# Kernel optimization log

Measured on AMD Instinct MI355X. Metric: run time of the kernel, lower is better.

The kernel has to match this reference:

```python
import jax, jax.numpy as jnp
import numpy as np

SHAPES = ((64, 64), (32, 32), (16, 16), (8, 8))
HEADS, LV, P = 8, 4, 8


def _ln(x, g, b, eps=1e-5):
    m = x.mean(-1, keepdims=True)
    v = ((x - m) ** 2).mean(-1, keepdims=True)
    return (x - m) * jax.lax.rsqrt(v + eps) * g + b


def _sample_level(v, H, W, loc):
    # v: [B, heads, H*W, hd] value for one level; loc: [B, L, heads, P, 2] in [0,1]
    # Matches F.grid_sample(mode='bilinear', padding_mode='zeros', align_corners=False)
    x = loc[..., 0] * W - 0.5
    y = loc[..., 1] * H - 0.5
    x0 = jnp.floor(x)
    y0 = jnp.floor(y)
    B, L, hds, Pn = x.shape
    acc = 0.0
    for dx, dy in ((0, 0), (1, 0), (0, 1), (1, 1)):
        xi = x0 + dx
        yi = y0 + dy
        w = (1.0 - jnp.abs(x - xi)) * (1.0 - jnp.abs(y - yi))
        valid = (xi >= 0) & (xi < W) & (yi >= 0) & (yi < H)
        idx = (jnp.clip(yi, 0, H - 1) * W + jnp.clip(xi, 0, W - 1)).astype(jnp.int32)
        idx_r = idx.transpose(0, 2, 1, 3).reshape(B, hds, L * Pn)  # [B,heads,L*P]
        g = jnp.take_along_axis(v, idx_r[..., None], axis=2)  # [B,heads,L*P,hd]
        g = g.reshape(B, hds, L, Pn, -1).transpose(0, 2, 1, 3, 4)  # [B,L,heads,P,hd]
        acc = acc + (w * valid.astype(w.dtype))[..., None] * g
    return acc


def setup_inputs() -> dict:
    key = jax.random.key(0)
    ks = iter(jax.random.split(key, 64))
    B, d, depth, dff = 2, 256, 6, 1024
    inp = {}
    for i, (H, W) in enumerate(SHAPES):
        inp[f"src{i}"] = jax.random.normal(next(ks), (B, d, H, W), jnp.float32)
        inp[f"pos{i}"] = jax.random.normal(next(ks), (B, d, H, W), jnp.float32)
    s = 0.02
    off_dim = HEADS * LV * P * 2  # 512
    aw_dim = HEADS * LV * P  # 256
    inp["level_embed"] = jax.random.normal(next(ks), (LV, d), jnp.float32)
    inp["W_off"] = jax.random.normal(next(ks), (depth, d, off_dim), jnp.float32) * s
    inp["b_off"] = jax.random.normal(next(ks), (depth, off_dim), jnp.float32) * 0.5
    inp["W_attn"] = jax.random.normal(next(ks), (depth, d, aw_dim), jnp.float32) * s
    inp["b_attn"] = jnp.zeros((depth, aw_dim), jnp.float32)
    inp["W_val"] = jax.random.normal(next(ks), (depth, d, d), jnp.float32) * s
    inp["b_val"] = jnp.zeros((depth, d), jnp.float32)
    inp["W_out"] = jax.random.normal(next(ks), (depth, d, d), jnp.float32) * s
    inp["b_out"] = jnp.zeros((depth, d), jnp.float32)
    inp["ln1_g"] = jnp.ones((depth, d), jnp.float32)
    inp["ln1_b"] = jnp.zeros((depth, d), jnp.float32)
    inp["W1"] = jax.random.normal(next(ks), (depth, d, dff), jnp.float32) * s
    inp["b1"] = jnp.zeros((depth, dff), jnp.float32)
    inp["W2"] = jax.random.normal(next(ks), (depth, dff, d), jnp.float32) * s
    inp["b2"] = jnp.zeros((depth, d), jnp.float32)
    inp["ln2_g"] = jnp.ones((depth, d), jnp.float32)
    inp["ln2_b"] = jnp.zeros((depth, d), jnp.float32)
    return inp


def reference(src0, src1, src2, src3, pos0, pos1, pos2, pos3, level_embed,
              W_off, b_off, W_attn, b_attn, W_val, b_val, W_out, b_out,
              ln1_g, ln1_b, W1, b1, W2, b2, ln2_g, ln2_b):
    srcs = [src0, src1, src2, src3]
    poss = [pos0, pos1, pos2, pos3]
    B, d = src0.shape[0], src0.shape[1]
    hd = d // HEADS
    # flatten multi-scale maps: [B, C, H, W] -> [B, H*W, C]
    src_flat = jnp.concatenate([s.reshape(B, d, -1).transpose(0, 2, 1) for s in srcs], 1)
    pos_flat = jnp.concatenate(
        [p.reshape(B, d, -1).transpose(0, 2, 1) + level_embed[i] for i, p in enumerate(poss)], 1)
    # reference points; masks are all-False so valid_ratios == 1 (same ref for every level)
    refs = []
    for (H, W) in SHAPES:
        gy, gx = jnp.meshgrid((jnp.arange(H) + 0.5) / H, (jnp.arange(W) + 0.5) / W, indexing='ij')
        refs.append(jnp.stack([gx.reshape(-1), gy.reshape(-1)], -1))
    ref = jnp.concatenate(refs, 0)  # [L, 2]
    norm = jnp.array([[W, H] for (H, W) in SHAPES], jnp.float32)  # [LV, 2] (W_, H_)
    sizes = [H * W for (H, W) in SHAPES]
    starts = np.cumsum([0] + sizes[:-1]).tolist()
    depth = W_off.shape[0]
    L = src_flat.shape[1]
    x = src_flat
    for i in range(depth):
        # pre-norm deformable self-attention; value comes from un-normed residual stream
        x2 = _ln(x, ln1_g[i], ln1_b[i])
        q = x2 + pos_flat
        off = (q @ W_off[i] + b_off[i]).reshape(B, L, HEADS, LV, P, 2)
        attn = jax.nn.softmax((q @ W_attn[i] + b_attn[i]).reshape(B, L, HEADS, LV * P), -1)
        attn = attn.reshape(B, L, HEADS, LV, P)
        val = (x @ W_val[i] + b_val[i]).reshape(B, L, HEADS, hd).transpose(0, 2, 1, 3)  # [B,heads,L,hd]
        loc = ref[None, :, None, None, None, :] + off / norm[None, None, None, :, None, :]
        out = 0.0
        for l, (H, W) in enumerate(SHAPES):
            vl = val[:, :, starts[l]:starts[l] + sizes[l]]
            sl = _sample_level(vl, H, W, loc[:, :, :, l])  # [B,L,heads,P,hd]
            out = out + (attn[:, :, :, l, :, None] * sl).sum(3)
        out = out.reshape(B, L, d) @ W_out[i] + b_out[i]
        x = x + out
        # pre-norm FFN with exact gelu (torch default)
        x2 = _ln(x, ln2_g[i], ln2_b[i])
        x = x + jax.nn.gelu(x2 @ W1[i] + b1[i], approximate=False) @ W2[i] + b2[i]
    return x
```

## Files before the change

kernel.cpp:

```cpp
#include <hip/hip_runtime.h>
#include <hip/hip_bf16.h>
#include <math.h>

#define L_TOK 5440
#define NTOK  10880
#define D     256

typedef __attribute__((ext_vector_type(8))) short short8;
typedef __attribute__((ext_vector_type(4))) short short4v;
typedef __attribute__((ext_vector_type(4))) float f32x4;

__device__ __forceinline__ short f2bf(float f) {
    __hip_bfloat16 h = __float2bfloat16(f);
    return __builtin_bit_cast(short, h);
}
__device__ __forceinline__ float bf2f(short s) {
    unsigned u = ((unsigned)(unsigned short)s) << 16;
    return __builtin_bit_cast(float, u);
}

#define GLL16(gp, lp) \
    __builtin_amdgcn_global_load_lds((const __attribute__((address_space(1))) void*)(gp), \
                                     (__attribute__((address_space(3))) void*)(lp), 16, 0, 0)

__global__ __launch_bounds__(256) void flat_kernel(
    const float* __restrict__ s, const float* __restrict__ p, const float* __restrict__ le,
    float* __restrict__ x, short* __restrict__ xb, float* __restrict__ pos,
    int HW, int start, int lv)
{
    __shared__ float ts[32][33], tp[32][33];
    int b = blockIdx.z, c0 = blockIdx.y * 32, pix0 = blockIdx.x * 32;
    int tx = threadIdx.x & 31, ty = threadIdx.x >> 5;
#pragma unroll
    for (int i = 0; i < 4; ++i) {
        int c = c0 + ty + i * 8;
        size_t gi = ((size_t)b * D + c) * HW + pix0 + tx;
        ts[ty + i * 8][tx] = s[gi];
        tp[ty + i * 8][tx] = p[gi];
    }
    __syncthreads();
#pragma unroll
    for (int i = 0; i < 4; ++i) {
        int pix = pix0 + ty + i * 8;
        size_t bl = (size_t)b * L_TOK + start + pix;
        int c = c0 + tx;
        float v = ts[tx][ty + i * 8];
        x[bl * D + c]   = v;
        xb[bl * D + c]  = f2bf(v);
        pos[bl * D + c] = tp[tx][ty + i * 8] + le[lv * D + c];
    }
}

__global__ __launch_bounds__(256) void wconv_kernel(
    const float* __restrict__ W, short* __restrict__ Wt, int K, int N,
    int dstride, int rowoff)
{
    __shared__ float tile[32][33];
    int d = blockIdx.z;
    int n0 = blockIdx.x * 32, k0 = blockIdx.y * 32;
    const float* Wd = W + (size_t)d * K * N;
    short* Wtd = Wt + (size_t)d * dstride + (size_t)rowoff * K;
    int tx = threadIdx.x & 31, ty = threadIdx.x >> 5;
#pragma unroll
    for (int i = 0; i < 4; ++i)
        tile[ty + i * 8][tx] = Wd[(size_t)(k0 + ty + i * 8) * N + n0 + tx];
    __syncthreads();
#pragma unroll
    for (int i = 0; i < 4; ++i)
        Wtd[(size_t)(n0 + ty + i * 8) * K + k0 + tx] = f2bf(tile[tx][ty + i * 8]);
}

__global__ __launch_bounds__(256) void bpack_kernel(
    const float* __restrict__ boff, const float* __restrict__ batt, float* __restrict__ bqa)
{
    int i = blockIdx.x * 256 + threadIdx.x;
    if (i >= 6 * 768) return;
    int d = i / 768, c = i - d * 768;
    bqa[i] = (c < 512) ? boff[d * 512 + c] : batt[d * 256 + c - 512];
}

__global__ __launch_bounds__(256) void ln_kernel(
    const float* __restrict__ x, const float* __restrict__ g, const float* __restrict__ bta,
    const float* __restrict__ pos, short* __restrict__ out)
{
    int wid = threadIdx.x >> 6, lane = threadIdx.x & 63;
    int m = blockIdx.x * 4 + wid;
    const float* xr = x + (size_t)m * D;
    float v[4];
#pragma unroll
    for (int i = 0; i < 4; ++i) v[i] = xr[lane + i * 64];
    float s = v[0] + v[1] + v[2] + v[3];
#pragma unroll
    for (int o = 32; o; o >>= 1) s += __shfl_xor(s, o);
    float mean = s * (1.0f / D);
    float sq = 0.0f;
#pragma unroll
    for (int i = 0; i < 4; ++i) { float d = v[i] - mean; sq += d * d; }
#pragma unroll
    for (int o = 32; o; o >>= 1) sq += __shfl_xor(sq, o);
    float rstd = rsqrtf(sq * (1.0f / D) + 1e-5f);
    short* orow = out + (size_t)m * D;
#pragma unroll
    for (int i = 0; i < 4; ++i) {
        int c = lane + i * 64;
        float o = (v[i] - mean) * rstd * g[c] + bta[c];
        if (pos) o += pos[(size_t)m * D + c];
        orow[c] = f2bf(o);
    }
}

template<int BN>
__device__ __forceinline__ void mm_body64(
    const short* __restrict__ A, const short* __restrict__ Wt,
    const float* __restrict__ bias, const float* __restrict__ resid,
    float* __restrict__ Cf, short* __restrict__ Cb,
    int row0, int col0, int K, int ldc, int act)
{
    constexpr int NW  = BN / 4;
    constexpr int NF  = NW / 16;
    constexpr int BCH = BN / 32;
    __shared__ __align__(16) short As[2][64 * 64];
    __shared__ __align__(16) short Bs[2][BN * 64];
    int tid = threadIdx.x, lane = tid & 63, w = tid >> 6;
    int l15 = lane & 15, l16 = lane >> 4;

    int a_off[4][2], b_off[NF][2];
#pragma unroll
    for (int m = 0; m < 4; ++m)
#pragma unroll
        for (int kk = 0; kk < 2; ++kk) {
            int ra = m * 16 + l15;
            a_off[m][kk] = ra * 64 + (((kk * 4 + l16) ^ (ra & 7)) << 3);
        }
#pragma unroll
    for (int n = 0; n < NF; ++n)
#pragma unroll
        for (int kk = 0; kk < 2; ++kk) {
            int rb = w * NW + n * 16 + l15;
            b_off[n][kk] = rb * 64 + (((kk * 4 + l16) ^ (rb & 7)) << 3);
        }

    int sg = (lane & 7) ^ ((lane >> 3) & 7);
    const short* ag = A  + (size_t)(row0 + w * 16 + (lane >> 3)) * K + sg * 8;
    const short* bg = Wt + (size_t)(col0 + w * NW + (lane >> 3)) * K + sg * 8;

    f32x4 acc[4][NF];
#pragma unroll
    for (int m = 0; m < 4; ++m)
#pragma unroll
        for (int n = 0; n < NF; ++n) acc[m][n] = (f32x4){0.f, 0.f, 0.f, 0.f};

    auto stage = [&](int buf, int kofs) {
#pragma unroll
        for (int c = 0; c < 2; ++c)
            GLL16(ag + (size_t)c * 8 * K + kofs, &As[buf][w * 1024 + c * 512]);
#pragma unroll
        for (int c = 0; c < BCH; ++c)
            GLL16(bg + (size_t)c * 8 * K + kofs, &Bs[buf][w * NW * 64 + c * 512]);
    };
    auto comp = [&](int buf) {
#pragma unroll
        for (int kk = 0; kk < 2; ++kk) {
            short8 af[4], bfr[NF];
#pragma unroll
            for (int m = 0; m < 4; ++m) af[m] = *(short8*)&As[buf][a_off[m][kk]];
#pragma unroll
            for (int n = 0; n < NF; ++n) bfr[n] = *(short8*)&Bs[buf][b_off[n][kk]];
#pragma unroll
            for (int m = 0; m < 4; ++m)
#pragma unroll
                for (int n = 0; n < NF; ++n)
                    acc[m][n] = __builtin_amdgcn_mfma_f32_16x16x32_bf16(af[m], bfr[n], acc[m][n], 0, 0, 0);
        }
    };

    stage(0, 0);
    __syncthreads();
    int cur = 0;
    for (int k0 = 64; k0 < K; k0 += 64) {
        stage(cur ^ 1, k0);
        comp(cur);
        __syncthreads();
        cur ^= 1;
    }
    comp(cur);

#pragma unroll
    for (int m = 0; m < 4; ++m) {
#pragma unroll
        for (int j = 0; j < 4; ++j) {
            int row = row0 + m * 16 + l16 * 4 + j;
#pragma unroll
            for (int n = 0; n < NF; ++n) {
                int col = col0 + w * NW + n * 16 + l15;
                float v = acc[m][n][j] + bias[col];
                if (act) v = 0.5f * v * (1.0f + erff(v * 0.70710678118654752f));
                if (resid) v += resid[(size_t)row * ldc + col];
                if (Cf) Cf[(size_t)row * ldc + col] = v;
                if (Cb) Cb[(size_t)row * ldc + col] = f2bf(v);
            }
        }
    }
}

template<int BN>
__global__ __launch_bounds__(256) void mm_kernel(
    const short* __restrict__ A, const short* __restrict__ Wt,
    const float* __restrict__ bias, const float* __restrict__ resid,
    float* __restrict__ Cf, short* __restrict__ Cb, int K, int ldc, int act)
{
    mm_body64<BN>(A, Wt, bias, resid, Cf, Cb, blockIdx.y * 64, blockIdx.x * BN, K, ldc, act);
}

__global__ __launch_bounds__(256) void mm2_kernel(
    const short* __restrict__ A1, const short* __restrict__ Wt1, const float* __restrict__ bias1,
    float* __restrict__ Cf1, int ldc1,
    const short* __restrict__ A2, const short* __restrict__ Wt2, const float* __restrict__ bias2,
    short* __restrict__ Cb2, int ldc2,
    int nx1, int K)
{
    const short *A, *Wt; const float* bias; float* Cf; short* Cb; int ldc, col0;
    if ((int)blockIdx.x < nx1) {
        A = A1; Wt = Wt1; bias = bias1; Cf = Cf1; Cb = nullptr; ldc = ldc1;
        col0 = blockIdx.x * 128;
    } else {
        A = A2; Wt = Wt2; bias = bias2; Cf = nullptr; Cb = Cb2; ldc = ldc2;
        col0 = (blockIdx.x - nx1) * 128;
    }
    mm_body64<128>(A, Wt, bias, nullptr, Cf, Cb, blockIdx.y * 64, col0, K, ldc, 0);
}

__global__ __launch_bounds__(256) void sample_kernel(
    const float* __restrict__ big, const short* __restrict__ val, short* __restrict__ out)
{
    __shared__ float sw[8 * 132];
    __shared__ int   si[8 * 132];
    int bl = blockIdx.x;
    int b = bl / L_TOK, l = bl - b * L_TOK;
    const float* row = big + (size_t)bl * 768;
    int t = threadIdx.x;
    {
        int head = t >> 5, lvp = t & 31, lv = lvp >> 3, p = lvp & 7;
        int lq, r;
        if (l < 4096)      { lq = 0; r = l;        }
        else if (l < 5120) { lq = 1; r = l - 4096; }
        else if (l < 5376) { lq = 2; r = l - 5120; }
        else               { lq = 3; r = l - 5376; }
        int sh = 6 - lq;
        float invSq = 1.0f / (float)(1 << sh);
        float refx = ((r & ((1 << sh) - 1)) + 0.5f) * invSq;
        float refy = ((r >> sh) + 0.5f) * invSq;
        int S = 64 >> lv;
        int start = (lv == 0) ? 0 : (lv == 1) ? 4096 : (lv == 2) ? 5120 : 5376;
        float Sf = (float)S;
        float logit = row[512 + head * 32 + lvp];
        float mx = logit;
#pragma unroll
        for (int o = 16; o; o >>= 1) mx = fmaxf(mx, __shfl_xor(mx, o));
        float e = __expf(logit - mx);
        float ssum = e;
#pragma unroll
        for (int o = 16; o; o >>= 1) ssum += __shfl_xor(ssum, o);
        float a = e / ssum;
        float ox = row[head * 64 + lv * 16 + p * 2 + 0];
        float oy = row[head * 64 + lv * 16 + p * 2 + 1];
        float X = refx * Sf + ox - 0.5f;
        float Y = refy * Sf + oy - 0.5f;
        float x0 = floorf(X), y0 = floorf(Y);
        float fx = X - x0, fy = Y - y0;
        int xi0 = (int)x0, yi0 = (int)y0;
        int qt = lvp >> 3, sidx = lvp & 7;
        int base_w = head * 132 + qt * 33 + sidx * 4;
#pragma unroll
        for (int tap = 0; tap < 4; ++tap) {
            int dx = tap & 1, dy = tap >> 1;
            int xi = xi0 + dx, yi = yi0 + dy;
            float wgt = (dx ? fx : 1.0f - fx) * (dy ? fy : 1.0f - fy);
            bool valid = (xi >= 0) && (xi < S) && (yi >= 0) && (yi < S);
            int xc = xi < 0 ? 0 : (xi > S - 1 ? S - 1 : xi);
            int yc = yi < 0 ? 0 : (yi > S - 1 ? S - 1 : yi);
            sw[base_w + tap] = valid ? wgt * a : 0.0f;
            si[base_w + tap] = start + yc * S + xc;
        }
    }
    __syncthreads();
    int h = t >> 5, sgp = (t >> 2) & 7, cg = t & 3;
    const short* vb = val + (size_t)b * L_TOK * D + h * 32 + cg * 8;
    float a0 = 0.f, a1 = 0.f, a2 = 0.f, a3 = 0.f;
    float a4 = 0.f, a5 = 0.f, a6 = 0.f, a7 = 0.f;
#pragma unroll
    for (int ss = 0; ss < 4; ++ss) {
        int base = h * 132 + ss * 33 + sgp * 4;
#pragma unroll
        for (int tap = 0; tap < 4; ++tap) {
            float wgt = sw[base + tap];
            int   idx = si[base + tap];
            const short8 g = *(const short8*)&vb[(size_t)idx * D];
            a0 += wgt * bf2f(g[0]); a1 += wgt * bf2f(g[1]);
            a2 += wgt * bf2f(g[2]); a3 += wgt * bf2f(g[3]);
            a4 += wgt * bf2f(g[4]); a5 += wgt * bf2f(g[5]);
            a6 += wgt * bf2f(g[6]); a7 += wgt * bf2f(g[7]);
        }
    }
#pragma unroll
    for (int o = 4; o <= 16; o <<= 1) {
        a0 += __shfl_xor(a0, o); a1 += __shfl_xor(a1, o);
        a2 += __shfl_xor(a2, o); a3 += __shfl_xor(a3, o);
        a4 += __shfl_xor(a4, o); a5 += __shfl_xor(a5, o);
        a6 += __shfl_xor(a6, o); a7 += __shfl_xor(a7, o);
    }
    if (sgp == 0) {
        short8 o;
        o[0] = f2bf(a0); o[1] = f2bf(a1); o[2] = f2bf(a2); o[3] = f2bf(a3);
        o[4] = f2bf(a4); o[5] = f2bf(a5); o[6] = f2bf(a6); o[7] = f2bf(a7);
        *(short8*)&out[(size_t)bl * D + h * 32 + cg * 8] = o;
    }
}

extern "C" void kernel_launch(void* const* d_in, const int* in_sizes, int n_in,
                              void* d_out, int out_size, void* d_ws, size_t ws_size,
                              hipStream_t stream)
{
    const float* s0    = (const float*)d_in[0];
    const float* p0    = (const float*)d_in[1];
    const float* s1    = (const float*)d_in[2];
    const float* p1    = (const float*)d_in[3];
    const float* s2    = (const float*)d_in[4];
    const float* p2    = (const float*)d_in[5];
    const float* s3    = (const float*)d_in[6];
    const float* p3    = (const float*)d_in[7];
    const float* lvl   = (const float*)d_in[8];
    const float* W_off = (const float*)d_in[9];
    const float* b_off = (const float*)d_in[10];
    const float* W_att = (const float*)d_in[11];
    const float* b_att = (const float*)d_in[12];
    const float* W_val = (const float*)d_in[13];
    const float* b_val = (const float*)d_in[14];
    const float* W_out = (const float*)d_in[15];
    const float* b_out = (const float*)d_in[16];
    const float* ln1g  = (const float*)d_in[17];
    const float* ln1b  = (const float*)d_in[18];
    const float* W1    = (const float*)d_in[19];
    const float* b1    = (const float*)d_in[20];
    const float* W2    = (const float*)d_in[21];
    const float* b2    = (const float*)d_in[22];
    const float* ln2g  = (const float*)d_in[23];
    const float* ln2b  = (const float*)d_in[24];

    const size_t S1 = (size_t)NTOK * D;
    float* xbuf = (float*)d_ws;
    float* pos  = xbuf + S1;
    float* big  = pos + S1;
    float* bqa  = big + 3 * S1;
    short* qbf   = (short*)(bqa + 6 * 768);
    short* x_bf  = qbf + S1;
    short* valbf = x_bf + S1;
    short* sampb = valbf + S1;
    short* hidbf = sampb + S1;
    short* wt_qa  = hidbf + 4 * S1;
    short* wt_val = wt_qa  + (size_t)6 * 768 * 256;
    short* wt_out = wt_val + (size_t)6 * 256 * 256;
    short* wt_1   = wt_out + (size_t)6 * 256 * 256;
    short* wt_2   = wt_1   + (size_t)6 * 1024 * 256;

    wconv_kernel<<<dim3(16, 8, 6), 256, 0, stream>>>(W_off, wt_qa, 256, 512, 768 * 256, 0);
    wconv_kernel<<<dim3(8, 8, 6),  256, 0, stream>>>(W_att, wt_qa, 256, 256, 768 * 256, 512);
    wconv_kernel<<<dim3(8, 8, 6),  256, 0, stream>>>(W_val, wt_val, 256, 256, 256 * 256, 0);
    wconv_kernel<<<dim3(8, 8, 6),  256, 0, stream>>>(W_out, wt_out, 256, 256, 256 * 256, 0);
    wconv_kernel<<<dim3(32, 8, 6), 256, 0, stream>>>(W1,    wt_1,   256, 1024, 1024 * 256, 0);
    wconv_kernel<<<dim3(8, 32, 6), 256, 0, stream>>>(W2,    wt_2,   1024, 256, 256 * 1024, 0);
    bpack_kernel<<<18, 256, 0, stream>>>(b_off, b_att, bqa);

    flat_kernel<<<dim3(128, 8, 2), 256, 0, stream>>>(s0, p0, lvl, xbuf, x_bf, pos, 4096, 0, 0);
    flat_kernel<<<dim3(32, 8, 2),  256, 0, stream>>>(s1, p1, lvl, xbuf, x_bf, pos, 1024, 4096, 1);
    flat_kernel<<<dim3(8, 8, 2),   256, 0, stream>>>(s2, p2, lvl, xbuf, x_bf, pos, 256, 5120, 2);
    flat_kernel<<<dim3(2, 8, 2),   256, 0, stream>>>(s3, p3, lvl, xbuf, x_bf, pos, 64, 5376, 3);

    for (int i = 0; i < 6; ++i) {
        ln_kernel<<<NTOK / 4, 256, 0, stream>>>(xbuf, ln1g + i * 256, ln1b + i * 256, pos, qbf);
        mm2_kernel<<<dim3(8, 170), 256, 0, stream>>>(
            qbf, wt_qa + (size_t)i * 768 * 256, bqa + i * 768, big, 768,
            x_bf, wt_val + (size_t)i * 256 * 256, b_val + i * 256, valbf, 256,
            6, 256);
        sample_kernel<<<NTOK, 256, 0, stream>>>(big, valbf, sampb);
        mm_kernel<64><<<dim3(4, 170), 256, 0, stream>>>(
            sampb, wt_out + (size_t)i * 256 * 256, b_out + i * 256, xbuf, xbuf, nullptr, 256, 256, 0);
        ln_kernel<<<NTOK / 4, 256, 0, stream>>>(xbuf, ln2g + i * 256, ln2b + i * 256, nullptr, qbf);
        mm_kernel<128><<<dim3(8, 170), 256, 0, stream>>>(
            qbf, wt_1 + (size_t)i * 1024 * 256, b1 + i * 1024, nullptr, nullptr, hidbf, 256, 1024, 1);
        float* outp = (i == 5) ? (float*)d_out : xbuf;
        short* xbp  = (i == 5) ? nullptr : x_bf;
        mm_kernel<64><<<dim3(4, 170), 256, 0, stream>>>(
            hidbf, wt_2 + (size_t)i * 256 * 1024, b2 + i * 256, xbuf, outp, xbp, 1024, 256, 0);
    }
}
```

Measured before the change: 793.6 us.

## Store offset/attention logits as fp16 and batch gathers in sampling kernel

The offset/attention projection output now goes out as fp16 instead of fp32, halving the bytes written by the GEMM and read by the sampling kernel. The sampler also prescales gather indices by the row stride and issues eight 16-byte gathers back to back before accumulating, to expose more memory-level parallelism. Storing offsets in fp16 loses precision in sampling locations, which could perturb the bilinear weights.

```diff
diff --git a/kernel.cpp b/kernel.cpp
--- a/kernel.cpp
+++ b/kernel.cpp
@@ -7,7 +7,6 @@
 #define D     256
 
 typedef __attribute__((ext_vector_type(8))) short short8;
-typedef __attribute__((ext_vector_type(4))) short short4v;
 typedef __attribute__((ext_vector_type(4))) float f32x4;
 
 __device__ __forceinline__ short f2bf(float f) {
@@ -114,7 +113,7 @@
     const short* __restrict__ A, const short* __restrict__ Wt,
     const float* __restrict__ bias, const float* __restrict__ resid,
     float* __restrict__ Cf, short* __restrict__ Cb,
-    int row0, int col0, int K, int ldc, int act)
+    int row0, int col0, int K, int ldc, int act, int f16out)
 {
     constexpr int NW  = BN / 4;
     constexpr int NF  = NW / 16;
@@ -197,7 +196,8 @@
                 if (act) v = 0.5f * v * (1.0f + erff(v * 0.70710678118654752f));
                 if (resid) v += resid[(size_t)row * ldc + col];
                 if (Cf) Cf[(size_t)row * ldc + col] = v;
-                if (Cb) Cb[(size_t)row * ldc + col] = f2bf(v);
+                if (Cb) Cb[(size_t)row * ldc + col] =
+                    f16out ? __builtin_bit_cast(short, (_Float16)v) : f2bf(v);
             }
         }
     }
@@ -209,35 +209,35 @@
     const float* __restrict__ bias, const float* __restrict__ resid,
     float* __restrict__ Cf, short* __restrict__ Cb, int K, int ldc, int act)
 {
-    mm_body64<BN>(A, Wt, bias, resid, Cf, Cb, blockIdx.y * 64, blockIdx.x * BN, K, ldc, act);
+    mm_body64<BN>(A, Wt, bias, resid, Cf, Cb, blockIdx.y * 64, blockIdx.x * BN, K, ldc, act, 0);
 }
 
 __global__ __launch_bounds__(256) void mm2_kernel(
     const short* __restrict__ A1, const short* __restrict__ Wt1, const float* __restrict__ bias1,
-    float* __restrict__ Cf1, int ldc1,
+    short* __restrict__ C1, int ldc1,
     const short* __restrict__ A2, const short* __restrict__ Wt2, const float* __restrict__ bias2,
-    short* __restrict__ Cb2, int ldc2,
+    short* __restrict__ C2, int ldc2,
     int nx1, int K)
 {
-    const short *A, *Wt; const float* bias; float* Cf; short* Cb; int ldc, col0;
+    const short *A, *Wt; const float* bias; short* Cb; int ldc, col0, f16o;
     if ((int)blockIdx.x < nx1) {
-        A = A1; Wt = Wt1; bias = bias1; Cf = Cf1; Cb = nullptr; ldc = ldc1;
+        A = A1; Wt = Wt1; bias = bias1; Cb = C1; ldc = ldc1; f16o = 1;
         col0 = blockIdx.x * 128;
     } else {
-        A = A2; Wt = Wt2; bias = bias2; Cf = nullptr; Cb = Cb2; ldc = ldc2;
+        A = A2; Wt = Wt2; bias = bias2; Cb = C2; ldc = ldc2; f16o = 0;
         col0 = (blockIdx.x - nx1) * 128;
     }
-    mm_body64<128>(A, Wt, bias, nullptr, Cf, Cb, blockIdx.y * 64, col0, K, ldc, 0);
+    mm_body64<128>(A, Wt, bias, nullptr, nullptr, Cb, blockIdx.y * 64, col0, K, ldc, 0, f16o);
 }
 
 __global__ __launch_bounds__(256) void sample_kernel(
-    const float* __restrict__ big, const short* __restrict__ val, short* __restrict__ out)
+    const short* __restrict__ big, const short* __restrict__ val, short* __restrict__ out)
 {
     __shared__ float sw[8 * 132];
     __shared__ int   si[8 * 132];
     int bl = blockIdx.x;
     int b = bl / L_TOK, l = bl - b * L_TOK;
-    const float* row = big + (size_t)bl * 768;
+    const _Float16* row = (const _Float16*)big + (size_t)bl * 768;
     int t = threadIdx.x;
     {
         int head = t >> 5, lvp = t & 31, lv = lvp >> 3, p = lvp & 7;
@@ -253,7 +253,7 @@
         int S = 64 >> lv;
         int start = (lv == 0) ? 0 : (lv == 1) ? 4096 : (lv == 2) ? 5120 : 5376;
         float Sf = (float)S;
-        float logit = row[512 + head * 32 + lvp];
+        float logit = (float)row[512 + head * 32 + lvp];
         float mx = logit;
 #pragma unroll
         for (int o = 16; o; o >>= 1) mx = fmaxf(mx, __shfl_xor(mx, o));
@@ -262,8 +262,8 @@
 #pragma unroll
         for (int o = 16; o; o >>= 1) ssum += __shfl_xor(ssum, o);
         float a = e / ssum;
-        float ox = row[head * 64 + lv * 16 + p * 2 + 0];
-        float oy = row[head * 64 + lv * 16 + p * 2 + 1];
+        float ox = (float)row[head * 64 + lv * 16 + p * 2 + 0];
+        float oy = (float)row[head * 64 + lv * 16 + p * 2 + 1];
         float X = refx * Sf + ox - 0.5f;
         float Y = refy * Sf + oy - 0.5f;
         float x0 = floorf(X), y0 = floorf(Y);
@@ -280,7 +280,7 @@
             int xc = xi < 0 ? 0 : (xi > S - 1 ? S - 1 : xi);
             int yc = yi < 0 ? 0 : (yi > S - 1 ? S - 1 : yi);
             sw[base_w + tap] = valid ? wgt * a : 0.0f;
-            si[base_w + tap] = start + yc * S + xc;
+            si[base_w + tap] = (start + yc * S + xc) << 8;
         }
     }
     __syncthreads();
@@ -289,17 +289,27 @@
     float a0 = 0.f, a1 = 0.f, a2 = 0.f, a3 = 0.f;
     float a4 = 0.f, a5 = 0.f, a6 = 0.f, a7 = 0.f;
 #pragma unroll
-    for (int ss = 0; ss < 4; ++ss) {
-        int base = h * 132 + ss * 33 + sgp * 4;
-#pragma unroll
-        for (int tap = 0; tap < 4; ++tap) {
-            float wgt = sw[base + tap];
-            int   idx = si[base + tap];
-            const short8 g = *(const short8*)&vb[(size_t)idx * D];
-            a0 += wgt * bf2f(g[0]); a1 += wgt * bf2f(g[1]);
-            a2 += wgt * bf2f(g[2]); a3 += wgt * bf2f(g[3]);
-            a4 += wgt * bf2f(g[4]); a5 += wgt * bf2f(g[5]);
-            a6 += wgt * bf2f(g[6]); a7 += wgt * bf2f(g[7]);
+    for (int gp = 0; gp < 2; ++gp) {
+        float w8[8]; int i8[8];
+#pragma unroll
+        for (int ss = 0; ss < 2; ++ss) {
+            int base = h * 132 + (gp * 2 + ss) * 33 + sgp * 4;
+#pragma unroll
+            for (int tap = 0; tap < 4; ++tap) {
+                w8[ss * 4 + tap] = sw[base + tap];
+                i8[ss * 4 + tap] = si[base + tap];
+            }
+        }
+        short8 g[8];
+#pragma unroll
+        for (int k = 0; k < 8; ++k) g[k] = *(const short8*)&vb[i8[k]];
+#pragma unroll
+        for (int k = 0; k < 8; ++k) {
+            float wgt = w8[k];
+            a0 += wgt * bf2f(g[k][0]); a1 += wgt * bf2f(g[k][1]);
+            a2 += wgt * bf2f(g[k][2]); a3 += wgt * bf2f(g[k][3]);
+            a4 += wgt * bf2f(g[k][4]); a5 += wgt * bf2f(g[k][5]);
+            a6 += wgt * bf2f(g[k][6]); a7 += wgt * bf2f(g[k][7]);
         }
     }
 #pragma unroll
@@ -350,8 +360,9 @@
     const size_t S1 = (size_t)NTOK * D;
     float* xbuf = (float*)d_ws;
     float* pos  = xbuf + S1;
-    float* big  = pos + S1;
-    float* bqa  = big + 3 * S1;
+    float* bigf = pos + S1;
+    float* bqa  = bigf + 3 * S1;
+    short* big  = (short*)bigf;
     short* qbf   = (short*)(bqa + 6 * 768);
     short* x_bf  = qbf + S1;
     short* valbf = x_bf + S1;
```

Measured after the change: 778.3 us. Within noise of the previous version (-1.9%).
